# Kernel tuning notes

Measured on AMD Instinct MI355X. Metric: run time of the kernel, lower is better.

## Reference

```python
import jax, jax.numpy as jnp
import numpy as np

N = 200_000      # nodes
E = 1_000_000    # edges
B = 4096         # source batch
K = 20           # n_neighbors
DN = 128         # n_node_features
DEMB = 128       # embedding_dimension (interval emb hidden)
DMEM = DN + DEMB # memory dim (forced by memory + cat(node_feat, delta_emb))
DT = 128         # n_time_features
DE = 128         # n_edge_features
NBINS = 300


def setup_inputs() -> dict:
    key = jax.random.key(0)
    ks = jax.random.split(key, 16)
    return {
        "node_features": jax.random.normal(ks[0], (N, DN), jnp.float32),
        "edge_features": jax.random.normal(ks[1], (E, DE), jnp.float32),
        "memory": jax.random.normal(ks[2], (N, DMEM), jnp.float32),
        "interval_table": jax.random.normal(ks[3], (NBINS, DEMB), jnp.float32),
        "bin_boundaries": jnp.linspace(0.0, 100.0, NBINS + 1).astype(jnp.float32),
        "time_w": jax.random.normal(ks[4], (DT,), jnp.float32),
        "time_b": jax.random.normal(ks[5], (DT,), jnp.float32),
        "W_agg": jax.random.normal(ks[6], (DT + DE, DMEM), jnp.float32) / np.sqrt(DT + DE),
        "timestamps": jax.random.uniform(ks[7], (B,), jnp.float32, 0.0, 100.0),
        "edge_times": jax.random.uniform(ks[8], (B, K), jnp.float32, 0.0, 100.0),
        "intervals": jax.random.uniform(ks[9], (B,), jnp.float32, 0.0, 100.0),
        "nei_intervals": jax.random.uniform(ks[10], (B, K), jnp.float32, 0.0, 100.0),
        "source_nodes": jax.random.randint(ks[11], (B,), 0, N),
        "neighbors": jax.random.randint(ks[12], (B, K), 0, N),
        "edge_idxs": jax.random.randint(ks[13], (B, K), 0, E),
    }


def reference(node_features, edge_features, memory, interval_table, bin_boundaries,
              time_w, time_b, W_agg, timestamps, edge_times, intervals,
              nei_intervals, source_nodes, neighbors, edge_idxs):
    # LearnableIntervalEmbedding.forward: bucketize -> clamp -> embedding lookup
    def interval_embed(x):
        idx = jnp.searchsorted(bin_boundaries, x, side='left') - 1  # torch.bucketize(right=False)
        idx = jnp.clip(idx, 0, NBINS - 1)
        return interval_table[idx]

    # TGN-style time encoder: cos(t * w + b)
    def time_enc(t):
        return jnp.cos(t[..., None] * time_w + time_b)

    # n_layers == 0 path: memory add + gather + interval embed + concat
    def layer0(idx, ivals):
        return memory[idx] + jnp.concatenate(
            [node_features[idx], interval_embed(ivals)], axis=-1)

    src0 = layer0(source_nodes, intervals)          # [B, DMEM]
    nb0 = layer0(neighbors, nei_intervals)          # [B, K, DMEM]

    edge_deltas = timestamps[:, None] - edge_times  # [B, K]
    ete = time_enc(edge_deltas)                     # [B, K, DT]
    ef = edge_features[edge_idxs]                   # [B, K, DE]
    # aggregate (abstract in source): masked mean of neighbor embeddings plus
    # linearly merged (edge_time_emb, edge_feat) messages, added to source emb.
    msg = jnp.einsum('bkf,fd->bkd', jnp.concatenate([ete, ef], axis=-1), W_agg)

    valid = (neighbors != -1)[..., None].astype(src0.dtype)  # mask = neighbors == -1
    cnt = jnp.maximum(valid.sum(axis=1), 1.0)
    out = src0 + (nb0 * valid).sum(axis=1) / cnt + (msg * valid).sum(axis=1) / cnt
    return out
```

## Files before the change

### kernel.cpp

```cpp
#include <hip/hip_runtime.h>
#include <math.h>

#define KN     20
#define DMEMC  256
#define DNC    128
#define DEC    128
#define DEMBC  128
#define NBINSC 300
#define MPB    4

__device__ __forceinline__ float4 ld4(const float* p) {
    return *reinterpret_cast<const float4*>(p);
}

__global__ __launch_bounds__(256) void graph_emb_kernel(
    const float* __restrict__ node_features,
    const float* __restrict__ edge_features,
    const float* __restrict__ memory_,
    const float* __restrict__ interval_table,
    const float* __restrict__ bin_boundaries,
    const float* __restrict__ time_w,
    const float* __restrict__ time_b,
    const float* __restrict__ W_agg,
    const float* __restrict__ timestamps,
    const float* __restrict__ edge_times,
    const float* __restrict__ intervals,
    const float* __restrict__ nei_intervals,
    const int*   __restrict__ source_nodes,
    const int*   __restrict__ neighbors,
    const int*   __restrict__ edge_idxs,
    float* __restrict__ out, int B)
{
    __shared__ float s_bb[NBINSC + 1];
    __shared__ __align__(16) float s_feat[MPB][DMEMC];
    __shared__ __align__(16) float s_res[MPB][DMEMC];
    __shared__ int s_bins[MPB][KN + 1];

    const int t  = threadIdx.x;
    const int w  = t >> 6;
    const int l  = t & 63;
    const int b0 = blockIdx.x * MPB;
    const int b  = b0 + w;

    for (int i = t; i <= NBINSC; i += 256) s_bb[i] = bin_boundaries[i];
    __syncthreads();

    if (l <= KN && b < B) {
        const float x = (l == 0) ? intervals[b] : nei_intervals[b * KN + (l - 1)];
        int lo = 0, hi = NBINSC + 1;
        while (lo < hi) {
            int mid = (lo + hi) >> 1;
            if (s_bb[mid] < x) lo = mid + 1; else hi = mid;
        }
        int idx = lo - 1;
        idx = idx < 0 ? 0 : (idx > NBINSC - 1 ? NBINSC - 1 : idx);
        s_bins[w][l] = idx;
    }
    __syncthreads();

    if (b < B) {
        float cnt = 0.f;
        #pragma unroll
        for (int k = 0; k < KN; ++k) cnt += (neighbors[b * KN + k] != -1) ? 1.f : 0.f;
        const float inv = 1.f / fmaxf(cnt, 1.f);

        const int d0 = 4 * l;

        const long src = source_nodes[b];
        float4 v = ld4(memory_ + src * DMEMC + d0);
        if (l < 32) {
            float4 a = ld4(node_features + src * DNC + d0);
            v.x += a.x; v.y += a.y; v.z += a.z; v.w += a.w;
        } else {
            float4 a = ld4(interval_table + (long)s_bins[w][0] * DEMBC + (d0 - 128));
            v.x += a.x; v.y += a.y; v.z += a.z; v.w += a.w;
        }
        float4 nb4 = make_float4(0.f, 0.f, 0.f, 0.f);
        #pragma unroll
        for (int k = 0; k < KN; ++k) {
            const int nb = neighbors[b * KN + k];
            if (nb != -1) {
                float4 x = ld4(memory_ + (long)nb * DMEMC + d0);
                float4 a;
                if (l < 32) a = ld4(node_features + (long)nb * DNC + d0);
                else        a = ld4(interval_table + (long)s_bins[w][k + 1] * DEMBC + (d0 - 128));
                nb4.x += x.x + a.x; nb4.y += x.y + a.y;
                nb4.z += x.z + a.z; nb4.w += x.w + a.w;
            }
        }
        float4 r = make_float4(v.x + nb4.x * inv, v.y + nb4.y * inv,
                               v.z + nb4.z * inv, v.w + nb4.w * inv);
        *reinterpret_cast<float4*>(&s_res[w][d0]) = r;

        float4 fs = make_float4(0.f, 0.f, 0.f, 0.f);
        if (l < 32) {
            const float4 w4 = ld4(time_w + d0);
            const float4 c4 = ld4(time_b + d0);
            const float ts = timestamps[b];
            #pragma unroll
            for (int k = 0; k < KN; ++k) {
                if (neighbors[b * KN + k] != -1) {
                    const float dlt = ts - edge_times[b * KN + k];
                    fs.x += __cosf(fmaf(dlt, w4.x, c4.x));
                    fs.y += __cosf(fmaf(dlt, w4.y, c4.y));
                    fs.z += __cosf(fmaf(dlt, w4.z, c4.z));
                    fs.w += __cosf(fmaf(dlt, w4.w, c4.w));
                }
            }
        } else {
            const int e0 = d0 - 128;
            #pragma unroll
            for (int k = 0; k < KN; ++k) {
                if (neighbors[b * KN + k] != -1) {
                    const long e = edge_idxs[b * KN + k];
                    float4 a = ld4(edge_features + e * DEC + e0);
                    fs.x += a.x; fs.y += a.y; fs.z += a.z; fs.w += a.w;
                }
            }
        }
        fs.x *= inv; fs.y *= inv; fs.z *= inv; fs.w *= inv;
        *reinterpret_cast<float4*>(&s_feat[w][d0]) = fs;
    }
    __syncthreads();

    float a0 = 0.f, a1 = 0.f, a2 = 0.f, a3 = 0.f;
    for (int f = 0; f < DMEMC; ++f) {
        const float wv = W_agg[f * DMEMC + t];
        a0 = fmaf(s_feat[0][f], wv, a0);
        a1 = fmaf(s_feat[1][f], wv, a1);
        a2 = fmaf(s_feat[2][f], wv, a2);
        a3 = fmaf(s_feat[3][f], wv, a3);
    }
    if (b0 + 0 < B) out[(long)(b0 + 0) * DMEMC + t] = s_res[0][t] + a0;
    if (b0 + 1 < B) out[(long)(b0 + 1) * DMEMC + t] = s_res[1][t] + a1;
    if (b0 + 2 < B) out[(long)(b0 + 2) * DMEMC + t] = s_res[2][t] + a2;
    if (b0 + 3 < B) out[(long)(b0 + 3) * DMEMC + t] = s_res[3][t] + a3;
}

extern "C" void kernel_launch(void* const* d_in, const int* in_sizes, int n_in,
                              void* d_out, int out_size, void* d_ws, size_t ws_size,
                              hipStream_t stream) {
    const float* node_features  = (const float*)d_in[0];
    const float* edge_features  = (const float*)d_in[1];
    const float* memory_        = (const float*)d_in[2];
    const float* interval_table = (const float*)d_in[3];
    const float* bin_boundaries = (const float*)d_in[4];
    const float* time_w         = (const float*)d_in[5];
    const float* time_b         = (const float*)d_in[6];
    const float* W_agg          = (const float*)d_in[7];
    const float* timestamps     = (const float*)d_in[8];
    const float* edge_times     = (const float*)d_in[9];
    const float* intervals      = (const float*)d_in[10];
    const float* nei_intervals  = (const float*)d_in[11];
    const int*   source_nodes   = (const int*)d_in[12];
    const int*   neighbors      = (const int*)d_in[13];
    const int*   edge_idxs      = (const int*)d_in[14];
    float* out = (float*)d_out;

    const int B = in_sizes[8];
    const int grid = (B + MPB - 1) / MPB;
    graph_emb_kernel<<<grid, 256, 0, stream>>>(
        node_features, edge_features, memory_, interval_table, bin_boundaries,
        time_w, time_b, W_agg, timestamps, edge_times, intervals, nei_intervals,
        source_nodes, neighbors, edge_idxs, out, B);
}
```

Before: 742.4 us.

## Fuse neighbor loops branch-free and split W_agg matvec across waves by K-slices

Merges the neighbor-embedding gather and edge/time feature loops into one unrolled loop. It uses a mask multiply and a clamped index instead of branches, and puts indices in scalar registers via readfirstlane. The W_agg projection is restructured so each wave takes a 64-row slice of the reduction dimension with float4 weight loads and register blocking. Partial sums go to shared memory and are reduced at the end. This trades extra LDS space and one more barrier for more memory-level parallelism and fewer scalar weight loads. It also issues gathers for masked neighbors using index 0.

```diff
diff --git a/kernel.cpp b/kernel.cpp
--- a/kernel.cpp
+++ b/kernel.cpp
@@ -12,6 +12,16 @@
 __device__ __forceinline__ float4 ld4(const float* p) {
     return *reinterpret_cast<const float4*>(p);
 }
+
+#define ACC4(acc, q, W0, W1, W2, W3)                                                   \
+    acc.x = fmaf(q.x, W0.x, acc.x); acc.x = fmaf(q.y, W1.x, acc.x);                    \
+    acc.x = fmaf(q.z, W2.x, acc.x); acc.x = fmaf(q.w, W3.x, acc.x);                    \
+    acc.y = fmaf(q.x, W0.y, acc.y); acc.y = fmaf(q.y, W1.y, acc.y);                    \
+    acc.y = fmaf(q.z, W2.y, acc.y); acc.y = fmaf(q.w, W3.y, acc.y);                    \
+    acc.z = fmaf(q.x, W0.z, acc.z); acc.z = fmaf(q.y, W1.z, acc.z);                    \
+    acc.z = fmaf(q.z, W2.z, acc.z); acc.z = fmaf(q.w, W3.z, acc.z);                    \
+    acc.w = fmaf(q.x, W0.w, acc.w); acc.w = fmaf(q.y, W1.w, acc.w);                    \
+    acc.w = fmaf(q.z, W2.w, acc.w); acc.w = fmaf(q.w, W3.w, acc.w);
 
 __global__ __launch_bounds__(256) void graph_emb_kernel(
     const float* __restrict__ node_features,
@@ -34,6 +44,7 @@
     __shared__ float s_bb[NBINSC + 1];
     __shared__ __align__(16) float s_feat[MPB][DMEMC];
     __shared__ __align__(16) float s_res[MPB][DMEMC];
+    __shared__ __align__(16) float s_part[4][MPB][DMEMC];
     __shared__ int s_bins[MPB][KN + 1];
 
     const int t  = threadIdx.x;
@@ -58,83 +69,108 @@
     }
     __syncthreads();
 
+    const int d0 = 4 * l;
     if (b < B) {
+        const int src = __builtin_amdgcn_readfirstlane(source_nodes[b]);
+        float4 v = ld4(memory_ + (long)src * DMEMC + d0);
+        float4 w4, c4;
+        float ts = 0.f;
+        if (l < 32) {
+            const float4 a = ld4(node_features + (long)src * DNC + d0);
+            v.x += a.x; v.y += a.y; v.z += a.z; v.w += a.w;
+            w4 = ld4(time_w + d0);
+            c4 = ld4(time_b + d0);
+            ts = timestamps[b];
+        } else {
+            const float4 a = ld4(interval_table + (long)s_bins[w][0] * DEMBC + (d0 - 128));
+            v.x += a.x; v.y += a.y; v.z += a.z; v.w += a.w;
+        }
+
         float cnt = 0.f;
-        #pragma unroll
-        for (int k = 0; k < KN; ++k) cnt += (neighbors[b * KN + k] != -1) ? 1.f : 0.f;
-        const float inv = 1.f / fmaxf(cnt, 1.f);
-
-        const int d0 = 4 * l;
-
-        const long src = source_nodes[b];
-        float4 v = ld4(memory_ + src * DMEMC + d0);
-        if (l < 32) {
-            float4 a = ld4(node_features + src * DNC + d0);
-            v.x += a.x; v.y += a.y; v.z += a.z; v.w += a.w;
-        } else {
-            float4 a = ld4(interval_table + (long)s_bins[w][0] * DEMBC + (d0 - 128));
-            v.x += a.x; v.y += a.y; v.z += a.z; v.w += a.w;
-        }
         float4 nb4 = make_float4(0.f, 0.f, 0.f, 0.f);
+        float4 fs  = make_float4(0.f, 0.f, 0.f, 0.f);
         #pragma unroll
         for (int k = 0; k < KN; ++k) {
-            const int nb = neighbors[b * KN + k];
-            if (nb != -1) {
-                float4 x = ld4(memory_ + (long)nb * DMEMC + d0);
-                float4 a;
-                if (l < 32) a = ld4(node_features + (long)nb * DNC + d0);
-                else        a = ld4(interval_table + (long)s_bins[w][k + 1] * DEMBC + (d0 - 128));
-                nb4.x += x.x + a.x; nb4.y += x.y + a.y;
-                nb4.z += x.z + a.z; nb4.w += x.w + a.w;
+            const int raw = __builtin_amdgcn_readfirstlane(neighbors[b * KN + k]);
+            const float msk = (raw != -1) ? 1.f : 0.f;
+            const int nbc = raw & ~(raw >> 31);
+            cnt += msk;
+
+            const float4 x = ld4(memory_ + (long)nbc * DMEMC + d0);
+            float4 a, f;
+            if (l < 32) {
+                a = ld4(node_features + (long)nbc * DNC + d0);
+                const float dlt = ts - edge_times[b * KN + k];
+                f.x = __cosf(fmaf(dlt, w4.x, c4.x));
+                f.y = __cosf(fmaf(dlt, w4.y, c4.y));
+                f.z = __cosf(fmaf(dlt, w4.z, c4.z));
+                f.w = __cosf(fmaf(dlt, w4.w, c4.w));
+            } else {
+                const int e0 = d0 - 128;
+                a = ld4(interval_table + (long)s_bins[w][k + 1] * DEMBC + e0);
+                int ei = __builtin_amdgcn_readfirstlane(edge_idxs[b * KN + k]);
+                ei = ei & ~(ei >> 31);
+                f = ld4(edge_features + (long)ei * DEC + e0);
             }
-        }
-        float4 r = make_float4(v.x + nb4.x * inv, v.y + nb4.y * inv,
-                               v.z + nb4.z * inv, v.w + nb4.w * inv);
+            nb4.x = fmaf(x.x + a.x, msk, nb4.x);
+            nb4.y = fmaf(x.y + a.y, msk, nb4.y);
+            nb4.z = fmaf(x.z + a.z, msk, nb4.z);
+            nb4.w = fmaf(x.w + a.w, msk, nb4.w);
+            fs.x  = fmaf(f.x, msk, fs.x);
+            fs.y  = fmaf(f.y, msk, fs.y);
+            fs.z  = fmaf(f.z, msk, fs.z);
+            fs.w  = fmaf(f.w, msk, fs.w);
+        }
+        const float inv = 1.f / fmaxf(cnt, 1.f);
+        float4 r;
+        r.x = fmaf(nb4.x, inv, v.x);
+        r.y = fmaf(nb4.y, inv, v.y);
+        r.z = fmaf(nb4.z, inv, v.z);
+        r.w = fmaf(nb4.w, inv, v.w);
         *reinterpret_cast<float4*>(&s_res[w][d0]) = r;
-
-        float4 fs = make_float4(0.f, 0.f, 0.f, 0.f);
-        if (l < 32) {
-            const float4 w4 = ld4(time_w + d0);
-            const float4 c4 = ld4(time_b + d0);
-            const float ts = timestamps[b];
-            #pragma unroll
-            for (int k = 0; k < KN; ++k) {
-                if (neighbors[b * KN + k] != -1) {
-                    const float dlt = ts - edge_times[b * KN + k];
-                    fs.x += __cosf(fmaf(dlt, w4.x, c4.x));
-                    fs.y += __cosf(fmaf(dlt, w4.y, c4.y));
-                    fs.z += __cosf(fmaf(dlt, w4.z, c4.z));
-                    fs.w += __cosf(fmaf(dlt, w4.w, c4.w));
-                }
-            }
-        } else {
-            const int e0 = d0 - 128;
-            #pragma unroll
-            for (int k = 0; k < KN; ++k) {
-                if (neighbors[b * KN + k] != -1) {
-                    const long e = edge_idxs[b * KN + k];
-                    float4 a = ld4(edge_features + e * DEC + e0);
-                    fs.x += a.x; fs.y += a.y; fs.z += a.z; fs.w += a.w;
-                }
-            }
-        }
         fs.x *= inv; fs.y *= inv; fs.z *= inv; fs.w *= inv;
         *reinterpret_cast<float4*>(&s_feat[w][d0]) = fs;
     }
     __syncthreads();
 
-    float a0 = 0.f, a1 = 0.f, a2 = 0.f, a3 = 0.f;
-    for (int f = 0; f < DMEMC; ++f) {
-        const float wv = W_agg[f * DMEMC + t];
-        a0 = fmaf(s_feat[0][f], wv, a0);
-        a1 = fmaf(s_feat[1][f], wv, a1);
-        a2 = fmaf(s_feat[2][f], wv, a2);
-        a3 = fmaf(s_feat[3][f], wv, a3);
-    }
-    if (b0 + 0 < B) out[(long)(b0 + 0) * DMEMC + t] = s_res[0][t] + a0;
-    if (b0 + 1 < B) out[(long)(b0 + 1) * DMEMC + t] = s_res[1][t] + a1;
-    if (b0 + 2 < B) out[(long)(b0 + 2) * DMEMC + t] = s_res[2][t] + a2;
-    if (b0 + 3 < B) out[(long)(b0 + 3) * DMEMC + t] = s_res[3][t] + a3;
+    {
+        const int f0 = w * 64;
+        float4 acc0 = make_float4(0.f, 0.f, 0.f, 0.f);
+        float4 acc1 = make_float4(0.f, 0.f, 0.f, 0.f);
+        float4 acc2 = make_float4(0.f, 0.f, 0.f, 0.f);
+        float4 acc3 = make_float4(0.f, 0.f, 0.f, 0.f);
+        #pragma unroll 2
+        for (int fg = 0; fg < 64; fg += 4) {
+            const int f = f0 + fg;
+            const float4 q0 = *reinterpret_cast<const float4*>(&s_feat[0][f]);
+            const float4 q1 = *reinterpret_cast<const float4*>(&s_feat[1][f]);
+            const float4 q2 = *reinterpret_cast<const float4*>(&s_feat[2][f]);
+            const float4 q3 = *reinterpret_cast<const float4*>(&s_feat[3][f]);
+            const float4 W0 = ld4(W_agg + (long)(f + 0) * DMEMC + d0);
+            const float4 W1 = ld4(W_agg + (long)(f + 1) * DMEMC + d0);
+            const float4 W2 = ld4(W_agg + (long)(f + 2) * DMEMC + d0);
+            const float4 W3 = ld4(W_agg + (long)(f + 3) * DMEMC + d0);
+            ACC4(acc0, q0, W0, W1, W2, W3);
+            ACC4(acc1, q1, W0, W1, W2, W3);
+            ACC4(acc2, q2, W0, W1, W2, W3);
+            ACC4(acc3, q3, W0, W1, W2, W3);
+        }
+        *reinterpret_cast<float4*>(&s_part[w][0][d0]) = acc0;
+        *reinterpret_cast<float4*>(&s_part[w][1][d0]) = acc1;
+        *reinterpret_cast<float4*>(&s_part[w][2][d0]) = acc2;
+        *reinterpret_cast<float4*>(&s_part[w][3][d0]) = acc3;
+    }
+    __syncthreads();
+
+    #pragma unroll
+    for (int s = 0; s < MPB; ++s) {
+        const int bb = b0 + s;
+        if (bb < B) {
+            out[(long)bb * DMEMC + t] = s_res[s][t]
+                + s_part[0][s][t] + s_part[1][s][t]
+                + s_part[2][s][t] + s_part[3][s][t];
+        }
+    }
 }
 
 extern "C" void kernel_launch(void* const* d_in, const int* in_sizes, int n_in,
```

Result: slower. 825.4 us (+11.2%).

## Split neighbor gather across two waves per sample and split-K the W_agg matvec

Applied to the files above, without the earlier changes.

Each block now handles two samples, with two wavefronts per sample, each gathering half of the 20 neighbors. Neighbor indices, edge times and edge indices are preloaded into registers to expose more memory-level parallelism. The W_agg projection is split over the feature dimension across the four waves using float4 weight loads, and the partial sums are reduced in shared memory. Normalization by the neighbor count is applied once at the end. This doubles the grid size and the W_agg reads per sample, and adds shared-memory traffic and an extra barrier.

```diff
diff --git a/kernel.cpp b/kernel.cpp
--- a/kernel.cpp
+++ b/kernel.cpp
@@ -2,16 +2,27 @@
 #include <math.h>
 
 #define KN     20
+#define HALF   10
 #define DMEMC  256
 #define DNC    128
 #define DEC    128
 #define DEMBC  128
 #define NBINSC 300
-#define MPB    4
+#define MPB    2
 
 __device__ __forceinline__ float4 ld4(const float* p) {
     return *reinterpret_cast<const float4*>(p);
 }
+
+#define ACC4(acc, q, W0, W1, W2, W3)                                                   \
+    acc.x = fmaf(q.x, W0.x, acc.x); acc.x = fmaf(q.y, W1.x, acc.x);                    \
+    acc.x = fmaf(q.z, W2.x, acc.x); acc.x = fmaf(q.w, W3.x, acc.x);                    \
+    acc.y = fmaf(q.x, W0.y, acc.y); acc.y = fmaf(q.y, W1.y, acc.y);                    \
+    acc.y = fmaf(q.z, W2.y, acc.y); acc.y = fmaf(q.w, W3.y, acc.y);                    \
+    acc.z = fmaf(q.x, W0.z, acc.z); acc.z = fmaf(q.y, W1.z, acc.z);                    \
+    acc.z = fmaf(q.z, W2.z, acc.z); acc.z = fmaf(q.w, W3.z, acc.z);                    \
+    acc.w = fmaf(q.x, W0.w, acc.w); acc.w = fmaf(q.y, W1.w, acc.w);                    \
+    acc.w = fmaf(q.z, W2.w, acc.w); acc.w = fmaf(q.w, W3.w, acc.w);
 
 __global__ __launch_bounds__(256) void graph_emb_kernel(
     const float* __restrict__ node_features,
@@ -32,20 +43,25 @@
     float* __restrict__ out, int B)
 {
     __shared__ float s_bb[NBINSC + 1];
-    __shared__ __align__(16) float s_feat[MPB][DMEMC];
-    __shared__ __align__(16) float s_res[MPB][DMEMC];
-    __shared__ int s_bins[MPB][KN + 1];
+    __shared__ int   s_bins[MPB][KN + 1];
+    __shared__ float s_cnt[MPB][2];
+    __shared__ __align__(16) float s_src[MPB][DMEMC];
+    __shared__ __align__(16) float s_gB[MPB][2][DMEMC];
+    __shared__ __align__(16) float s_gA[MPB][2][DMEMC];
+    __shared__ __align__(16) float s_part[4][MPB][DMEMC];
 
     const int t  = threadIdx.x;
     const int w  = t >> 6;
     const int l  = t & 63;
+    const int s  = w >> 1;
+    const int h  = w & 1;
     const int b0 = blockIdx.x * MPB;
-    const int b  = b0 + w;
+    const int b  = b0 + s;
 
     for (int i = t; i <= NBINSC; i += 256) s_bb[i] = bin_boundaries[i];
     __syncthreads();
 
-    if (l <= KN && b < B) {
+    if (h == 0 && l <= KN && b < B) {
         const float x = (l == 0) ? intervals[b] : nei_intervals[b * KN + (l - 1)];
         int lo = 0, hi = NBINSC + 1;
         while (lo < hi) {
@@ -54,53 +70,60 @@
         }
         int idx = lo - 1;
         idx = idx < 0 ? 0 : (idx > NBINSC - 1 ? NBINSC - 1 : idx);
-        s_bins[w][l] = idx;
-    }
-    __syncthreads();
-
+        s_bins[s][l] = idx;
+    }
+    __syncthreads();
+
+    const int d0 = 4 * l;
     if (b < B) {
+        const int kb0 = h * HALF;
+
+        int nbk[HALF];
+        #pragma unroll
+        for (int k = 0; k < HALF; ++k) nbk[k] = neighbors[b * KN + kb0 + k];
+
         float cnt = 0.f;
         #pragma unroll
-        for (int k = 0; k < KN; ++k) cnt += (neighbors[b * KN + k] != -1) ? 1.f : 0.f;
-        const float inv = 1.f / fmaxf(cnt, 1.f);
-
-        const int d0 = 4 * l;
-
-        const long src = source_nodes[b];
-        float4 v = ld4(memory_ + src * DMEMC + d0);
-        if (l < 32) {
-            float4 a = ld4(node_features + src * DNC + d0);
-            v.x += a.x; v.y += a.y; v.z += a.z; v.w += a.w;
-        } else {
-            float4 a = ld4(interval_table + (long)s_bins[w][0] * DEMBC + (d0 - 128));
-            v.x += a.x; v.y += a.y; v.z += a.z; v.w += a.w;
-        }
+        for (int k = 0; k < HALF; ++k) cnt += (nbk[k] != -1) ? 1.f : 0.f;
+        if (l == 0) s_cnt[s][h] = cnt;
+
         float4 nb4 = make_float4(0.f, 0.f, 0.f, 0.f);
         #pragma unroll
-        for (int k = 0; k < KN; ++k) {
-            const int nb = neighbors[b * KN + k];
+        for (int k = 0; k < HALF; ++k) {
+            const int nb = nbk[k];
             if (nb != -1) {
-                float4 x = ld4(memory_ + (long)nb * DMEMC + d0);
+                const float4 x = ld4(memory_ + (long)nb * DMEMC + d0);
                 float4 a;
                 if (l < 32) a = ld4(node_features + (long)nb * DNC + d0);
-                else        a = ld4(interval_table + (long)s_bins[w][k + 1] * DEMBC + (d0 - 128));
+                else        a = ld4(interval_table + (long)s_bins[s][kb0 + k + 1] * DEMBC + (d0 - 128));
                 nb4.x += x.x + a.x; nb4.y += x.y + a.y;
                 nb4.z += x.z + a.z; nb4.w += x.w + a.w;
             }
         }
-        float4 r = make_float4(v.x + nb4.x * inv, v.y + nb4.y * inv,
-                               v.z + nb4.z * inv, v.w + nb4.w * inv);
-        *reinterpret_cast<float4*>(&s_res[w][d0]) = r;
+        *reinterpret_cast<float4*>(&s_gB[s][h][d0]) = nb4;
+
+        if (h == 0) {
+            const int src = source_nodes[b];
+            float4 v = ld4(memory_ + (long)src * DMEMC + d0);
+            float4 a;
+            if (l < 32) a = ld4(node_features + (long)src * DNC + d0);
+            else        a = ld4(interval_table + (long)s_bins[s][0] * DEMBC + (d0 - 128));
+            v.x += a.x; v.y += a.y; v.z += a.z; v.w += a.w;
+            *reinterpret_cast<float4*>(&s_src[s][d0]) = v;
+        }
 
         float4 fs = make_float4(0.f, 0.f, 0.f, 0.f);
         if (l < 32) {
             const float4 w4 = ld4(time_w + d0);
             const float4 c4 = ld4(time_b + d0);
             const float ts = timestamps[b];
-            #pragma unroll
-            for (int k = 0; k < KN; ++k) {
-                if (neighbors[b * KN + k] != -1) {
-                    const float dlt = ts - edge_times[b * KN + k];
+            float et[HALF];
+            #pragma unroll
+            for (int k = 0; k < HALF; ++k) et[k] = edge_times[b * KN + kb0 + k];
+            #pragma unroll
+            for (int k = 0; k < HALF; ++k) {
+                if (nbk[k] != -1) {
+                    const float dlt = ts - et[k];
                     fs.x += __cosf(fmaf(dlt, w4.x, c4.x));
                     fs.y += __cosf(fmaf(dlt, w4.y, c4.y));
                     fs.z += __cosf(fmaf(dlt, w4.z, c4.z));
@@ -109,32 +132,59 @@
             }
         } else {
             const int e0 = d0 - 128;
-            #pragma unroll
-            for (int k = 0; k < KN; ++k) {
-                if (neighbors[b * KN + k] != -1) {
-                    const long e = edge_idxs[b * KN + k];
-                    float4 a = ld4(edge_features + e * DEC + e0);
+            int eik[HALF];
+            #pragma unroll
+            for (int k = 0; k < HALF; ++k) eik[k] = edge_idxs[b * KN + kb0 + k];
+            #pragma unroll
+            for (int k = 0; k < HALF; ++k) {
+                if (nbk[k] != -1) {
+                    const float4 a = ld4(edge_features + (long)eik[k] * DEC + e0);
                     fs.x += a.x; fs.y += a.y; fs.z += a.z; fs.w += a.w;
                 }
             }
         }
-        fs.x *= inv; fs.y *= inv; fs.z *= inv; fs.w *= inv;
-        *reinterpret_cast<float4*>(&s_feat[w][d0]) = fs;
-    }
-    __syncthreads();
-
-    float a0 = 0.f, a1 = 0.f, a2 = 0.f, a3 = 0.f;
-    for (int f = 0; f < DMEMC; ++f) {
-        const float wv = W_agg[f * DMEMC + t];
-        a0 = fmaf(s_feat[0][f], wv, a0);
-        a1 = fmaf(s_feat[1][f], wv, a1);
-        a2 = fmaf(s_feat[2][f], wv, a2);
-        a3 = fmaf(s_feat[3][f], wv, a3);
-    }
-    if (b0 + 0 < B) out[(long)(b0 + 0) * DMEMC + t] = s_res[0][t] + a0;
-    if (b0 + 1 < B) out[(long)(b0 + 1) * DMEMC + t] = s_res[1][t] + a1;
-    if (b0 + 2 < B) out[(long)(b0 + 2) * DMEMC + t] = s_res[2][t] + a2;
-    if (b0 + 3 < B) out[(long)(b0 + 3) * DMEMC + t] = s_res[3][t] + a3;
+        *reinterpret_cast<float4*>(&s_gA[s][h][d0]) = fs;
+    }
+    __syncthreads();
+
+    {
+        const int f0 = w * 64;
+        float4 acc0 = make_float4(0.f, 0.f, 0.f, 0.f);
+        float4 acc1 = make_float4(0.f, 0.f, 0.f, 0.f);
+        #pragma unroll 2
+        for (int fg = 0; fg < 64; fg += 4) {
+            const int f = f0 + fg;
+            const float4 qa0 = *reinterpret_cast<const float4*>(&s_gA[0][0][f]);
+            const float4 qb0 = *reinterpret_cast<const float4*>(&s_gA[0][1][f]);
+            const float4 qa1 = *reinterpret_cast<const float4*>(&s_gA[1][0][f]);
+            const float4 qb1 = *reinterpret_cast<const float4*>(&s_gA[1][1][f]);
+            const float4 q0 = make_float4(qa0.x + qb0.x, qa0.y + qb0.y,
+                                          qa0.z + qb0.z, qa0.w + qb0.w);
+            const float4 q1 = make_float4(qa1.x + qb1.x, qa1.y + qb1.y,
+                                          qa1.z + qb1.z, qa1.w + qb1.w);
+            const float4 W0 = ld4(W_agg + (long)(f + 0) * DMEMC + d0);
+            const float4 W1 = ld4(W_agg + (long)(f + 1) * DMEMC + d0);
+            const float4 W2 = ld4(W_agg + (long)(f + 2) * DMEMC + d0);
+            const float4 W3 = ld4(W_agg + (long)(f + 3) * DMEMC + d0);
+            ACC4(acc0, q0, W0, W1, W2, W3);
+            ACC4(acc1, q1, W0, W1, W2, W3);
+        }
+        *reinterpret_cast<float4*>(&s_part[w][0][d0]) = acc0;
+        *reinterpret_cast<float4*>(&s_part[w][1][d0]) = acc1;
+    }
+    __syncthreads();
+
+    #pragma unroll
+    for (int ss = 0; ss < MPB; ++ss) {
+        const int bb = b0 + ss;
+        if (bb < B) {
+            const float inv = 1.f / fmaxf(s_cnt[ss][0] + s_cnt[ss][1], 1.f);
+            const float gB = s_gB[ss][0][t] + s_gB[ss][1][t];
+            const float pa = s_part[0][ss][t] + s_part[1][ss][t]
+                           + s_part[2][ss][t] + s_part[3][ss][t];
+            out[(long)bb * DMEMC + t] = s_src[ss][t] + (gB + pa) * inv;
+        }
+    }
 }
 
 extern "C" void kernel_launch(void* const* d_in, const int* in_sizes, int n_in,
```

After: 745.2 us. No clear change (+0.4%).
